# Kernel tuning notes

Measured on AMD Instinct MI355X. Metric: run time of the kernel, lower is better.

Reference implementation:

```python
import jax, jax.numpy as jnp
import numpy as np

D_MODEL = 1024
HEADS = 16
SEQ = 2048
BATCH = 4
NEG_INF = -1e9
LN_EPS = 1e-5


def setup_inputs() -> dict:
    key = jax.random.key(0)
    ks = jax.random.split(key, 10)
    B, S, D = BATCH, SEQ, D_MODEL
    # xavier_uniform bound for square D x D linear
    bound = np.sqrt(6.0 / (D + D))
    def xavier(k):
        return jax.random.uniform(k, (D, D), jnp.float32, -bound, bound)
    return {
        "q": jax.random.normal(ks[0], (B, S, D), jnp.float32),
        "k": jax.random.normal(ks[1], (B, S, D), jnp.float32),
        "v": jax.random.normal(ks[2], (B, S, D), jnp.float32),
        "Wq": xavier(ks[3]),
        "Wk": xavier(ks[4]),
        "Wv": xavier(ks[5]),
        "Wo": xavier(ks[6]),
        "ln_gamma": jnp.ones((D,), jnp.float32),
        "ln_beta": jnp.zeros((D,), jnp.float32),
        "sen_len": jax.random.randint(ks[7], (B,), 1, S + 1, jnp.int32),
    }


def reference(q, k, v, Wq, Wk, Wv, Wo, ln_gamma, ln_beta, sen_len):
    B, S, D = q.shape
    H = HEADS
    d = D // H
    residual = q
    # projections (Linear with weight W applies x @ W.T)
    qh = jnp.einsum('bsd,ed->bse', q, Wq).reshape(B, S, H, d).transpose(0, 2, 1, 3)
    kh = jnp.einsum('bsd,ed->bse', k, Wk).reshape(B, S, H, d).transpose(0, 2, 1, 3)
    vh = jnp.einsum('bsd,ed->bse', v, Wv).reshape(B, S, H, d).transpose(0, 2, 1, 3)
    # scores [B,H,S,S]
    scores = jnp.einsum('bhqd,bhkd->bhqk', qh, kh) / np.sqrt(d).astype(np.float32)
    # padding mask on keys: j >= sen_len[b]; causal mask: j > i
    pad = jnp.arange(S)[None, :] >= sen_len[:, None]          # [B, S]
    causal = jnp.triu(jnp.ones((S, S), bool), 1)               # [S, S]
    mask = pad[:, None, None, :] | causal[None, None, :, :]
    scores = jnp.where(mask, NEG_INF, scores)
    att = jax.nn.softmax(scores, axis=-1)
    ctx = jnp.einsum('bhqk,bhkd->bhqd', att, vh)               # [B,H,S,d]
    ctx = ctx.transpose(0, 2, 1, 3).reshape(B, S, D)
    out = jnp.einsum('bsd,ed->bse', ctx, Wo)
    out = out + residual
    mean = out.mean(-1, keepdims=True)
    var = out.var(-1, keepdims=True)
    out = (out - mean) * jax.lax.rsqrt(var + LN_EPS) * ln_gamma + ln_beta
    return out
```

## Files before the change

### kernel.cpp

```cpp
#include <hip/hip_runtime.h>

typedef __bf16 bf16;
typedef bf16 bf16x8 __attribute__((ext_vector_type(8)));
typedef bf16 bf16x4 __attribute__((ext_vector_type(4)));
typedef float f32x4 __attribute__((ext_vector_type(4)));

#define ASYNC16(gp, lp) __builtin_amdgcn_global_load_lds( \
    (__attribute__((address_space(1))) void*)(const void*)(gp), \
    (__attribute__((address_space(3))) void*)(lp), 16, 0, 0)

__device__ __forceinline__ bf16x8 cvt2(const float4 a, const float4 b) {
    bf16x8 t;
    t[0] = (bf16)a.x; t[1] = (bf16)a.y; t[2] = (bf16)a.z; t[3] = (bf16)a.w;
    t[4] = (bf16)b.x; t[5] = (bf16)b.y; t[6] = (bf16)b.z; t[7] = (bf16)b.w;
    return t;
}

__global__ __launch_bounds__(256)
void cvt_w1(const float* __restrict__ W, bf16* __restrict__ out)
{
    const int i = blockIdx.x * 256 + threadIdx.x;
    const float4 a = ((const float4*)W)[i * 2];
    const float4 b = ((const float4*)W)[i * 2 + 1];
    *(bf16x8*)&out[(size_t)i * 8] = cvt2(a, b);
}

__global__ __launch_bounds__(256)
void cvt_w3(const float* __restrict__ W0, const float* __restrict__ W1,
            const float* __restrict__ W2, bf16* __restrict__ out)
{
    const int z = blockIdx.y;
    const float* src = (z == 0) ? W0 : (z == 1) ? W1 : W2;
    const int i = blockIdx.x * 256 + threadIdx.x;
    const float4 a = ((const float4*)src)[i * 2];
    const float4 b = ((const float4*)src)[i * 2 + 1];
    *(bf16x8*)&out[((size_t)z << 20) + (size_t)i * 8] = cvt2(a, b);
}

__global__ __launch_bounds__(256, 2)
void proj_gemm(const bf16* __restrict__ qb, const bf16* __restrict__ kb,
               const float* __restrict__ Av, const bf16* __restrict__ Wb3,
               bf16* __restrict__ Qp, bf16* __restrict__ Kp, bf16* __restrict__ Vt)
{
    constexpr int K = 1024;
    constexpr int BK = 32;
    __shared__ __align__(16) bf16 As[128 * BK];
    __shared__ __align__(16) bf16 Bs[128 * BK];

    const int z = blockIdx.z;
    const bf16* W = Wb3 + ((size_t)z << 20);

    const int tid  = threadIdx.x;
    const int lane = tid & 63;
    const int w    = tid >> 6;
    const int wr   = w >> 1, wc = w & 1;
    const int flat = blockIdx.y * 8 + blockIdx.x;
    const int m0   = (flat & 63) * 128;
    const int n0   = (flat >> 6) * 128;

    const bf16* Ab = (z == 0) ? qb : kb;

    f32x4 acc[4][4] = {};

    for (int k0 = 0; k0 < K; k0 += BK) {
        #pragma unroll
        for (int i = 0; i < 2; ++i) {
            const int c   = w * 128 + i * 64 + lane;
            const int row = c >> 2, kg = c & 3;
            ASYNC16(W + (size_t)(n0 + row) * K + k0 + kg * 8, &Bs[c * 8]);
            if (z < 2) {
                ASYNC16(Ab + (size_t)(m0 + row) * K + k0 + kg * 8, &As[c * 8]);
            } else {
                const float* ap = Av + (size_t)(m0 + row) * K + k0 + kg * 8;
                *(bf16x8*)&As[c * 8] = cvt2(*(const float4*)ap, *(const float4*)(ap + 4));
            }
        }
        __syncthreads();
        bf16x8 af[4], bfr[4];
        #pragma unroll
        for (int t = 0; t < 4; ++t) {
            af[t]  = *(const bf16x8*)&As[(wr * 64 + t * 16 + (lane & 15)) * BK + (lane >> 4) * 8];
            bfr[t] = *(const bf16x8*)&Bs[(wc * 64 + t * 16 + (lane & 15)) * BK + (lane >> 4) * 8];
        }
        #pragma unroll
        for (int mt = 0; mt < 4; ++mt)
            #pragma unroll
            for (int nt = 0; nt < 4; ++nt)
                acc[mt][nt] = __builtin_amdgcn_mfma_f32_16x16x32_bf16(af[mt], bfr[nt], acc[mt][nt], 0, 0, 0);
        __syncthreads();
    }

    #pragma unroll
    for (int mt = 0; mt < 4; ++mt) {
        #pragma unroll
        for (int nt = 0; nt < 4; ++nt) {
            const int mbase = m0 + wr * 64 + mt * 16 + ((lane >> 4) << 2);
            const int n     = n0 + wc * 64 + nt * 16 + (lane & 15);
            const int h = n >> 6, dd = n & 63;
            if (z < 2) {
                bf16* out = (z == 0) ? Qp : Kp;
                #pragma unroll
                for (int r = 0; r < 4; ++r) {
                    const int m = mbase + r;
                    const int b = m >> 11, s = m & 2047;
                    out[(((size_t)(b * 16 + h)) * 2048 + s) * 64 + dd] = (bf16)acc[mt][nt][r];
                }
            } else {
                const int b = mbase >> 11, s = mbase & 2047;
                bf16x4 v4;
                #pragma unroll
                for (int r = 0; r < 4; ++r) v4[r] = (bf16)acc[mt][nt][r];
                *(bf16x4*)&Vt[(((size_t)(b * 16 + h)) * 64 + dd) * 2048 + s] = v4;
            }
        }
    }
}

__global__ __launch_bounds__(256, 2)
void gemm_out(const bf16* __restrict__ A, const bf16* __restrict__ W,
              const float* __restrict__ R, float* __restrict__ out)
{
    constexpr int K = 1024;
    constexpr int BK = 32;
    __shared__ __align__(16) bf16 As[128 * BK];
    __shared__ __align__(16) bf16 Bs[128 * BK];

    const int tid  = threadIdx.x;
    const int lane = tid & 63;
    const int w    = tid >> 6;
    const int wr   = w >> 1, wc = w & 1;
    const int flat = blockIdx.y * 8 + blockIdx.x;
    const int m0   = (flat & 63) * 128;
    const int n0   = (flat >> 6) * 128;

    f32x4 acc[4][4] = {};

    for (int k0 = 0; k0 < K; k0 += BK) {
        #pragma unroll
        for (int i = 0; i < 2; ++i) {
            const int c   = w * 128 + i * 64 + lane;
            const int row = c >> 2, kg = c & 3;
            ASYNC16(A + (size_t)(m0 + row) * K + k0 + kg * 8, &As[c * 8]);
            ASYNC16(W + (size_t)(n0 + row) * K + k0 + kg * 8, &Bs[c * 8]);
        }
        __syncthreads();
        bf16x8 af[4], bfr[4];
        #pragma unroll
        for (int t = 0; t < 4; ++t) {
            af[t]  = *(const bf16x8*)&As[(wr * 64 + t * 16 + (lane & 15)) * BK + (lane >> 4) * 8];
            bfr[t] = *(const bf16x8*)&Bs[(wc * 64 + t * 16 + (lane & 15)) * BK + (lane >> 4) * 8];
        }
        #pragma unroll
        for (int mt = 0; mt < 4; ++mt)
            #pragma unroll
            for (int nt = 0; nt < 4; ++nt)
                acc[mt][nt] = __builtin_amdgcn_mfma_f32_16x16x32_bf16(af[mt], bfr[nt], acc[mt][nt], 0, 0, 0);
        __syncthreads();
    }

    #pragma unroll
    for (int mt = 0; mt < 4; ++mt) {
        #pragma unroll
        for (int nt = 0; nt < 4; ++nt) {
            const int mbase = m0 + wr * 64 + mt * 16 + ((lane >> 4) << 2);
            const int n     = n0 + wc * 64 + nt * 16 + (lane & 15);
            #pragma unroll
            for (int r = 0; r < 4; ++r) {
                const size_t idx = (size_t)(mbase + r) * 1024 + n;
                out[idx] = acc[mt][nt][r] + R[idx];
            }
        }
    }
}

__global__ __launch_bounds__(256, 2)
void attn_kernel(const bf16* __restrict__ Qp, const bf16* __restrict__ Kp,
                 const bf16* __restrict__ Vt, const int* __restrict__ sen_len,
                 bf16* __restrict__ ctx)
{
    const int qt = gridDim.x - 1 - blockIdx.x;
    const int h = blockIdx.y, b = blockIdx.z;
    const int q0 = qt * 128;
    const int bh = b * 16 + h;
    const int slen = sen_len[b];
    const int tid = threadIdx.x, lane = tid & 63, w = tid >> 6;
    const int wr = w >> 1, wc = w & 1;
    const float SCALE = 0.125f;
    const float SHIFT = 20.0f;

    __shared__ __align__(16) bf16 Ps[128 * 136];
    __shared__ float psum[2][128];

    bf16x8 qf[4][2];
    const bf16* Qbase = Qp + ((size_t)bh * 2048 + q0) * 64;
    #pragma unroll
    for (int mt = 0; mt < 4; ++mt)
        #pragma unroll
        for (int kk = 0; kk < 2; ++kk)
            qf[mt][kk] = *(const bf16x8*)(Qbase + (wr * 64 + mt * 16 + (lane & 15)) * 64
                                          + kk * 32 + (lane >> 4) * 8);

    f32x4 o[4][2] = {};
    float lsum[4][4] = {};

    const int jlim = min(q0 + 128, slen);
    const int nkt  = (jlim + 127) >> 7;

    const bf16* Kbh = Kp + (size_t)bh * 2048 * 64;
    const bf16* Vbh = Vt + (size_t)bh * 64 * 2048;

    for (int kt = 0; kt < nkt; ++kt) {
        const int k0 = kt * 128;

        f32x4 sf[4][4] = {};
        #pragma unroll
        for (int kk = 0; kk < 2; ++kk) {
            bf16x8 bk[4];
            #pragma unroll
            for (int nt = 0; nt < 4; ++nt)
                bk[nt] = *(const bf16x8*)(Kbh + (size_t)(k0 + wc * 64 + nt * 16 + (lane & 15)) * 64
                                          + kk * 32 + (lane >> 4) * 8);
            #pragma unroll
            for (int mt = 0; mt < 4; ++mt)
                #pragma unroll
                for (int nt = 0; nt < 4; ++nt)
                    sf[mt][nt] = __builtin_amdgcn_mfma_f32_16x16x32_bf16(qf[mt][kk], bk[nt], sf[mt][nt], 0, 0, 0);
        }

        if (kt == nkt - 1) {
            #pragma unroll
            for (int mt = 0; mt < 4; ++mt)
                #pragma unroll
                for (int r = 0; r < 4; ++r) {
                    const int row = wr * 64 + mt * 16 + ((lane >> 4) << 2) + r;
                    const int ig = q0 + row;
                    #pragma unroll
                    for (int nt = 0; nt < 4; ++nt) {
                        const int jg = k0 + wc * 64 + nt * 16 + (lane & 15);
                        const float sv = (jg > ig || jg >= slen) ? -1.0e9f : sf[mt][nt][r];
                        const float p = __expf(fmaf(sv, SCALE, -SHIFT));
                        lsum[mt][r] += p;
                        Ps[row * 136 + wc * 64 + nt * 16 + (lane & 15)] = (bf16)p;
                    }
                }
        } else {
            #pragma unroll
            for (int mt = 0; mt < 4; ++mt)
                #pragma unroll
                for (int r = 0; r < 4; ++r) {
                    const int row = wr * 64 + mt * 16 + ((lane >> 4) << 2) + r;
                    #pragma unroll
                    for (int nt = 0; nt < 4; ++nt) {
                        const float p = __expf(fmaf(sf[mt][nt][r], SCALE, -SHIFT));
                        lsum[mt][r] += p;
                        Ps[row * 136 + wc * 64 + nt * 16 + (lane & 15)] = (bf16)p;
                    }
                }
        }
        __syncthreads();

        #pragma unroll
        for (int ks = 0; ks < 4; ++ks) {
            bf16x8 pf[4], vf[2];
            #pragma unroll
            for (int mt = 0; mt < 4; ++mt)
                pf[mt] = *(const bf16x8*)&Ps[(wr * 64 + mt * 16 + (lane & 15)) * 136
                                             + ks * 32 + (lane >> 4) * 8];
            #pragma unroll
            for (int nt = 0; nt < 2; ++nt)
                vf[nt] = *(const bf16x8*)(Vbh + (size_t)(wc * 32 + nt * 16 + (lane & 15)) * 2048
                                          + k0 + ks * 32 + (lane >> 4) * 8);
            #pragma unroll
            for (int mt = 0; mt < 4; ++mt)
                #pragma unroll
                for (int nt = 0; nt < 2; ++nt)
                    o[mt][nt] = __builtin_amdgcn_mfma_f32_16x16x32_bf16(pf[mt], vf[nt], o[mt][nt], 0, 0, 0);
        }
        __syncthreads();
    }

    #pragma unroll
    for (int off = 1; off < 16; off <<= 1)
        #pragma unroll
        for (int mt = 0; mt < 4; ++mt)
            #pragma unroll
            for (int r = 0; r < 4; ++r)
                lsum[mt][r] += __shfl_xor(lsum[mt][r], off, 64);
    if ((lane & 15) == 0)
        #pragma unroll
        for (int mt = 0; mt < 4; ++mt)
            #pragma unroll
            for (int r = 0; r < 4; ++r)
                psum[wc][wr * 64 + mt * 16 + ((lane >> 4) << 2) + r] = lsum[mt][r];
    __syncthreads();

    #pragma unroll
    for (int mt = 0; mt < 4; ++mt)
        #pragma unroll
        for (int r = 0; r < 4; ++r) {
            const int row = wr * 64 + mt * 16 + ((lane >> 4) << 2) + r;
            const float inv = 1.0f / (psum[0][row] + psum[1][row]);
            const int sg = q0 + row;
            #pragma unroll
            for (int nt = 0; nt < 2; ++nt) {
                const int dd = wc * 32 + nt * 16 + (lane & 15);
                ctx[((size_t)(b * 2048 + sg)) * 1024 + h * 64 + dd] = (bf16)(o[mt][nt][r] * inv);
            }
        }
}

__global__ __launch_bounds__(256)
void ln_kernel(const float* __restrict__ y, const float* __restrict__ gamma,
               const float* __restrict__ beta, float* __restrict__ out)
{
    const int row = blockIdx.x;
    const int tid = threadIdx.x;
    const float4 v = ((const float4*)(y + (size_t)row * 1024))[tid];
    float s  = v.x + v.y + v.z + v.w;
    float s2 = v.x * v.x + v.y * v.y + v.z * v.z + v.w * v.w;
    #pragma unroll
    for (int o = 32; o > 0; o >>= 1) {
        s  += __shfl_down(s, o, 64);
        s2 += __shfl_down(s2, o, 64);
    }
    __shared__ float ps[4], ps2[4], stat[2];
    const int w = tid >> 6, lane = tid & 63;
    if (lane == 0) { ps[w] = s; ps2[w] = s2; }
    __syncthreads();
    if (tid == 0) {
        const float S  = ps[0] + ps[1] + ps[2] + ps[3];
        const float S2 = ps2[0] + ps2[1] + ps2[2] + ps2[3];
        const float mean = S * (1.0f / 1024.0f);
        const float var  = S2 * (1.0f / 1024.0f) - mean * mean;
        stat[0] = mean;
        stat[1] = rsqrtf(var + 1e-5f);
    }
    __syncthreads();
    const float mean = stat[0], rstd = stat[1];
    const float4 g4 = ((const float4*)gamma)[tid];
    const float4 b4 = ((const float4*)beta)[tid];
    float4 ov;
    ov.x = (v.x - mean) * rstd * g4.x + b4.x;
    ov.y = (v.y - mean) * rstd * g4.y + b4.y;
    ov.z = (v.z - mean) * rstd * g4.z + b4.z;
    ov.w = (v.w - mean) * rstd * g4.w + b4.w;
    ((float4*)(out + (size_t)row * 1024))[tid] = ov;
}

extern "C" void kernel_launch(void* const* d_in, const int* in_sizes, int n_in,
                              void* d_out, int out_size, void* d_ws, size_t ws_size,
                              hipStream_t stream)
{
    const float* q     = (const float*)d_in[0];
    const float* k     = (const float*)d_in[1];
    const float* v     = (const float*)d_in[2];
    const float* Wq    = (const float*)d_in[3];
    const float* Wk    = (const float*)d_in[4];
    const float* Wv    = (const float*)d_in[5];
    const float* Wo    = (const float*)d_in[6];
    const float* gamma = (const float*)d_in[7];
    const float* beta  = (const float*)d_in[8];
    const int*   sen   = (const int*)d_in[9];

    char* ws = (char*)d_ws;
    char* ob = (char*)d_out;
    const size_t SEG = 16777216;
    bf16* qb  = (bf16*)ob;
    bf16* kb  = (bf16*)(ob + SEG);
    bf16* ctx = (bf16*)ob;
    bf16* Qp  = (bf16*)(ws);
    bf16* Kp  = (bf16*)(ws + SEG);
    bf16* Vt  = (bf16*)(ws + 2 * SEG);
    bf16* Wb3 = (bf16*)(ws + 3 * SEG);
    bf16* WoB = (bf16*)(ws + 3 * SEG);
    float* y  = (float*)ws;

    dim3 bb(256);
    cvt_w1<<<dim3(4096), bb, 0, stream>>>(q, qb);
    cvt_w1<<<dim3(4096), bb, 0, stream>>>(k, kb);
    cvt_w3<<<dim3(512, 3), bb, 0, stream>>>(Wq, Wk, Wv, Wb3);
    proj_gemm<<<dim3(8, 64, 3), bb, 0, stream>>>(qb, kb, v, Wb3, Qp, Kp, Vt);
    attn_kernel<<<dim3(16, 16, 4), bb, 0, stream>>>(Qp, Kp, Vt, sen, ctx);
    cvt_w1<<<dim3(512), bb, 0, stream>>>(Wo, WoB);
    gemm_out<<<dim3(8, 64), bb, 0, stream>>>(ctx, WoB, q, y);
    ln_kernel<<<dim3(8192), bb, 0, stream>>>(y, gamma, beta, (float*)d_out);
}
```

Before: 352.6 us.

## Fuse q/k fp32-to-bf16 conversion into projection GEMM and widen K step

Drops the two standalone conversion kernels for q and k; the projection GEMM now reads fp32 activations for all three inputs and converts them to bf16 in registers before storing to LDS. Both GEMMs load 64 K-columns per barrier pair (two 32-wide LDS halves), halving the number of syncs. Q and K projections are written in plain row-major [B,S,D] layout, and the attention kernel indexes them with a 1024 stride. This saves a full read and write pass over q and k, but the GEMM A-tile loads become synchronous fp32 loads instead of async LDS copies.

```diff
diff --git a/kernel.cpp b/kernel.cpp
--- a/kernel.cpp
+++ b/kernel.cpp
@@ -38,16 +38,16 @@
 }
 
 __global__ __launch_bounds__(256, 2)
-void proj_gemm(const bf16* __restrict__ qb, const bf16* __restrict__ kb,
-               const float* __restrict__ Av, const bf16* __restrict__ Wb3,
+void proj_gemm(const float* __restrict__ q, const float* __restrict__ k,
+               const float* __restrict__ v, const bf16* __restrict__ Wb3,
                bf16* __restrict__ Qp, bf16* __restrict__ Kp, bf16* __restrict__ Vt)
 {
     constexpr int K = 1024;
-    constexpr int BK = 32;
-    __shared__ __align__(16) bf16 As[128 * BK];
-    __shared__ __align__(16) bf16 Bs[128 * BK];
+    __shared__ __align__(16) bf16 As[2][128 * 32];
+    __shared__ __align__(16) bf16 Bs[2][128 * 32];
 
     const int z = blockIdx.z;
+    const float* A = (z == 0) ? q : (z == 1) ? k : v;
     const bf16* W = Wb3 + ((size_t)z << 20);
 
     const int tid  = threadIdx.x;
@@ -58,35 +58,36 @@
     const int m0   = (flat & 63) * 128;
     const int n0   = (flat >> 6) * 128;
 
-    const bf16* Ab = (z == 0) ? qb : kb;
-
     f32x4 acc[4][4] = {};
 
-    for (int k0 = 0; k0 < K; k0 += BK) {
-        #pragma unroll
-        for (int i = 0; i < 2; ++i) {
-            const int c   = w * 128 + i * 64 + lane;
-            const int row = c >> 2, kg = c & 3;
-            ASYNC16(W + (size_t)(n0 + row) * K + k0 + kg * 8, &Bs[c * 8]);
-            if (z < 2) {
-                ASYNC16(Ab + (size_t)(m0 + row) * K + k0 + kg * 8, &As[c * 8]);
-            } else {
-                const float* ap = Av + (size_t)(m0 + row) * K + k0 + kg * 8;
-                *(bf16x8*)&As[c * 8] = cvt2(*(const float4*)ap, *(const float4*)(ap + 4));
-            }
-        }
-        __syncthreads();
-        bf16x8 af[4], bfr[4];
-        #pragma unroll
-        for (int t = 0; t < 4; ++t) {
-            af[t]  = *(const bf16x8*)&As[(wr * 64 + t * 16 + (lane & 15)) * BK + (lane >> 4) * 8];
-            bfr[t] = *(const bf16x8*)&Bs[(wc * 64 + t * 16 + (lane & 15)) * BK + (lane >> 4) * 8];
-        }
-        #pragma unroll
-        for (int mt = 0; mt < 4; ++mt)
-            #pragma unroll
-            for (int nt = 0; nt < 4; ++nt)
-                acc[mt][nt] = __builtin_amdgcn_mfma_f32_16x16x32_bf16(af[mt], bfr[nt], acc[mt][nt], 0, 0, 0);
+    for (int k0 = 0; k0 < K; k0 += 64) {
+        #pragma unroll
+        for (int half = 0; half < 2; ++half) {
+            #pragma unroll
+            for (int i = 0; i < 2; ++i) {
+                const int c   = w * 128 + i * 64 + lane;
+                const int row = c >> 2, kg = c & 3;
+                const int kb  = k0 + half * 32 + kg * 8;
+                ASYNC16(W + (size_t)(n0 + row) * K + kb, &Bs[half][c * 8]);
+                const float* ap = A + (size_t)(m0 + row) * K + kb;
+                *(bf16x8*)&As[half][c * 8] = cvt2(*(const float4*)ap, *(const float4*)(ap + 4));
+            }
+        }
+        __syncthreads();
+        #pragma unroll
+        for (int kk = 0; kk < 2; ++kk) {
+            bf16x8 af[4], bfr[4];
+            #pragma unroll
+            for (int t = 0; t < 4; ++t) {
+                af[t]  = *(const bf16x8*)&As[kk][(wr * 64 + t * 16 + (lane & 15)) * 32 + (lane >> 4) * 8];
+                bfr[t] = *(const bf16x8*)&Bs[kk][(wc * 64 + t * 16 + (lane & 15)) * 32 + (lane >> 4) * 8];
+            }
+            #pragma unroll
+            for (int mt = 0; mt < 4; ++mt)
+                #pragma unroll
+                for (int nt = 0; nt < 4; ++nt)
+                    acc[mt][nt] = __builtin_amdgcn_mfma_f32_16x16x32_bf16(af[mt], bfr[nt], acc[mt][nt], 0, 0, 0);
+        }
         __syncthreads();
     }
 
@@ -96,16 +97,13 @@
         for (int nt = 0; nt < 4; ++nt) {
             const int mbase = m0 + wr * 64 + mt * 16 + ((lane >> 4) << 2);
             const int n     = n0 + wc * 64 + nt * 16 + (lane & 15);
-            const int h = n >> 6, dd = n & 63;
             if (z < 2) {
                 bf16* out = (z == 0) ? Qp : Kp;
                 #pragma unroll
-                for (int r = 0; r < 4; ++r) {
-                    const int m = mbase + r;
-                    const int b = m >> 11, s = m & 2047;
-                    out[(((size_t)(b * 16 + h)) * 2048 + s) * 64 + dd] = (bf16)acc[mt][nt][r];
-                }
+                for (int r = 0; r < 4; ++r)
+                    out[(size_t)(mbase + r) * 1024 + n] = (bf16)acc[mt][nt][r];
             } else {
+                const int h = n >> 6, dd = n & 63;
                 const int b = mbase >> 11, s = mbase & 2047;
                 bf16x4 v4;
                 #pragma unroll
@@ -121,9 +119,8 @@
               const float* __restrict__ R, float* __restrict__ out)
 {
     constexpr int K = 1024;
-    constexpr int BK = 32;
-    __shared__ __align__(16) bf16 As[128 * BK];
-    __shared__ __align__(16) bf16 Bs[128 * BK];
+    __shared__ __align__(16) bf16 As[2][128 * 32];
+    __shared__ __align__(16) bf16 Bs[2][128 * 32];
 
     const int tid  = threadIdx.x;
     const int lane = tid & 63;
@@ -135,26 +132,33 @@
 
     f32x4 acc[4][4] = {};
 
-    for (int k0 = 0; k0 < K; k0 += BK) {
-        #pragma unroll
-        for (int i = 0; i < 2; ++i) {
-            const int c   = w * 128 + i * 64 + lane;
-            const int row = c >> 2, kg = c & 3;
-            ASYNC16(A + (size_t)(m0 + row) * K + k0 + kg * 8, &As[c * 8]);
-            ASYNC16(W + (size_t)(n0 + row) * K + k0 + kg * 8, &Bs[c * 8]);
-        }
-        __syncthreads();
-        bf16x8 af[4], bfr[4];
-        #pragma unroll
-        for (int t = 0; t < 4; ++t) {
-            af[t]  = *(const bf16x8*)&As[(wr * 64 + t * 16 + (lane & 15)) * BK + (lane >> 4) * 8];
-            bfr[t] = *(const bf16x8*)&Bs[(wc * 64 + t * 16 + (lane & 15)) * BK + (lane >> 4) * 8];
-        }
-        #pragma unroll
-        for (int mt = 0; mt < 4; ++mt)
-            #pragma unroll
-            for (int nt = 0; nt < 4; ++nt)
-                acc[mt][nt] = __builtin_amdgcn_mfma_f32_16x16x32_bf16(af[mt], bfr[nt], acc[mt][nt], 0, 0, 0);
+    for (int k0 = 0; k0 < K; k0 += 64) {
+        #pragma unroll
+        for (int half = 0; half < 2; ++half) {
+            #pragma unroll
+            for (int i = 0; i < 2; ++i) {
+                const int c   = w * 128 + i * 64 + lane;
+                const int row = c >> 2, kg = c & 3;
+                const int kb  = k0 + half * 32 + kg * 8;
+                ASYNC16(A + (size_t)(m0 + row) * K + kb, &As[half][c * 8]);
+                ASYNC16(W + (size_t)(n0 + row) * K + kb, &Bs[half][c * 8]);
+            }
+        }
+        __syncthreads();
+        #pragma unroll
+        for (int kk = 0; kk < 2; ++kk) {
+            bf16x8 af[4], bfr[4];
+            #pragma unroll
+            for (int t = 0; t < 4; ++t) {
+                af[t]  = *(const bf16x8*)&As[kk][(wr * 64 + t * 16 + (lane & 15)) * 32 + (lane >> 4) * 8];
+                bfr[t] = *(const bf16x8*)&Bs[kk][(wc * 64 + t * 16 + (lane & 15)) * 32 + (lane >> 4) * 8];
+            }
+            #pragma unroll
+            for (int mt = 0; mt < 4; ++mt)
+                #pragma unroll
+                for (int nt = 0; nt < 4; ++nt)
+                    acc[mt][nt] = __builtin_amdgcn_mfma_f32_16x16x32_bf16(af[mt], bfr[nt], acc[mt][nt], 0, 0, 0);
+        }
         __syncthreads();
     }
 
@@ -181,7 +185,6 @@
     const int qt = gridDim.x - 1 - blockIdx.x;
     const int h = blockIdx.y, b = blockIdx.z;
     const int q0 = qt * 128;
-    const int bh = b * 16 + h;
     const int slen = sen_len[b];
     const int tid = threadIdx.x, lane = tid & 63, w = tid >> 6;
     const int wr = w >> 1, wc = w & 1;
@@ -192,12 +195,12 @@
     __shared__ float psum[2][128];
 
     bf16x8 qf[4][2];
-    const bf16* Qbase = Qp + ((size_t)bh * 2048 + q0) * 64;
+    const bf16* Qbase = Qp + ((size_t)(b * 2048 + q0)) * 1024 + h * 64;
     #pragma unroll
     for (int mt = 0; mt < 4; ++mt)
         #pragma unroll
         for (int kk = 0; kk < 2; ++kk)
-            qf[mt][kk] = *(const bf16x8*)(Qbase + (wr * 64 + mt * 16 + (lane & 15)) * 64
+            qf[mt][kk] = *(const bf16x8*)(Qbase + (size_t)(wr * 64 + mt * 16 + (lane & 15)) * 1024
                                           + kk * 32 + (lane >> 4) * 8);
 
     f32x4 o[4][2] = {};
@@ -206,8 +209,8 @@
     const int jlim = min(q0 + 128, slen);
     const int nkt  = (jlim + 127) >> 7;
 
-    const bf16* Kbh = Kp + (size_t)bh * 2048 * 64;
-    const bf16* Vbh = Vt + (size_t)bh * 64 * 2048;
+    const bf16* Kbh = Kp + (size_t)b * 2048 * 1024 + h * 64;
+    const bf16* Vbh = Vt + (size_t)(b * 16 + h) * 64 * 2048;
 
     for (int kt = 0; kt < nkt; ++kt) {
         const int k0 = kt * 128;
@@ -218,7 +221,7 @@
             bf16x8 bk[4];
             #pragma unroll
             for (int nt = 0; nt < 4; ++nt)
-                bk[nt] = *(const bf16x8*)(Kbh + (size_t)(k0 + wc * 64 + nt * 16 + (lane & 15)) * 64
+                bk[nt] = *(const bf16x8*)(Kbh + (size_t)(k0 + wc * 64 + nt * 16 + (lane & 15)) * 1024
                                           + kk * 32 + (lane >> 4) * 8);
             #pragma unroll
             for (int mt = 0; mt < 4; ++mt)
@@ -363,23 +366,18 @@
     const int*   sen   = (const int*)d_in[9];
 
     char* ws = (char*)d_ws;
-    char* ob = (char*)d_out;
     const size_t SEG = 16777216;
-    bf16* qb  = (bf16*)ob;
-    bf16* kb  = (bf16*)(ob + SEG);
-    bf16* ctx = (bf16*)ob;
     bf16* Qp  = (bf16*)(ws);
     bf16* Kp  = (bf16*)(ws + SEG);
     bf16* Vt  = (bf16*)(ws + 2 * SEG);
     bf16* Wb3 = (bf16*)(ws + 3 * SEG);
     bf16* WoB = (bf16*)(ws + 3 * SEG);
     float* y  = (float*)ws;
+    bf16* ctx = (bf16*)d_out;
 
     dim3 bb(256);
-    cvt_w1<<<dim3(4096), bb, 0, stream>>>(q, qb);
-    cvt_w1<<<dim3(4096), bb, 0, stream>>>(k, kb);
     cvt_w3<<<dim3(512, 3), bb, 0, stream>>>(Wq, Wk, Wv, Wb3);
-    proj_gemm<<<dim3(8, 64, 3), bb, 0, stream>>>(qb, kb, v, Wb3, Qp, Kp, Vt);
+    proj_gemm<<<dim3(8, 64, 3), bb, 0, stream>>>(q, k, v, Wb3, Qp, Kp, Vt);
     attn_kernel<<<dim3(16, 16, 4), bb, 0, stream>>>(Qp, Kp, Vt, sen, ctx);
     cvt_w1<<<dim3(512), bb, 0, stream>>>(Wo, WoB);
     gemm_out<<<dim3(8, 64), bb, 0, stream>>>(ctx, WoB, q, y);
```

After: 315.2 us. -10.6%, faster.
